# Performance work log

Hardware: AMD Instinct MI355X
Metric: run time of the kernel (lower is better)

The kernel has to match this reference:

```python
import jax, jax.numpy as jnp
import numpy as np

N = 50000      # num_nodes
E = 800000     # num_edges
D = 128        # hidden_dim
POOL_RATIO = 0.5
CROSS_W = 1.0  # cross_weight


def _gcn(x, W, b, src, dst, n):
    """GCNConv: symmetric-normalized aggregation with self-loops. Dropout is identity (eval)."""
    loops = jnp.arange(n)
    s = jnp.concatenate([src, loops])
    d = jnp.concatenate([dst, loops])
    deg = jax.ops.segment_sum(jnp.ones(s.shape, x.dtype), d, num_segments=n)
    inv_sqrt = jax.lax.rsqrt(jnp.maximum(deg, 1.0))  # deg >= 1 due to self-loops
    xw = x @ W                                        # [n, D]
    msg = xw[s] * (inv_sqrt[s] * inv_sqrt[d])[:, None]  # [E+n, D] gather
    return jax.ops.segment_sum(msg, d, num_segments=n) + b


def _prelu(x, a):
    return jnp.where(x >= 0, x, a * x)


def setup_inputs() -> dict:
    key = jax.random.key(0)
    ks = jax.random.split(key, 8)
    glorot = lambda k, sh: jax.random.normal(k, sh, jnp.float32) * np.float32(np.sqrt(2.0 / (sh[0] + sh[1])))
    return {
        "feat": jax.random.normal(ks[0], (N, D), jnp.float32),
        "h_neg": jax.random.normal(ks[1], (N, D), jnp.float32),
        "edge_index": jax.random.randint(ks[2], (2, E), 0, N),
        "Wd": glorot(ks[3], (D, D)),
        "bd": jnp.zeros((D,), jnp.float32),
        "prelu_a": jnp.full((1,), 0.25, jnp.float32),
        "Wbil": glorot(ks[4], (D, D)),
        "bbil": jnp.zeros((1,), jnp.float32),
        "Wg1": glorot(ks[5], (D, D)),
        "bg1": jnp.zeros((D,), jnp.float32),
        "Wg2": glorot(ks[6], (D, D)),
        "bg2": jnp.zeros((D,), jnp.float32),
        "Wg3": glorot(ks[7], (D, D)),
        "bg3": jnp.zeros((D,), jnp.float32),
    }


def reference(feat, h_neg, edge_index, Wd, bd, prelu_a, Wbil, bbil,
              Wg1, bg1, Wg2, bg2, Wg3, bg3):
    src, dst = edge_index[0], edge_index[1]
    # --- IndexSelect: dense layer on pos/neg features ---
    h_pos = _prelu(feat @ Wd + bd, prelu_a)
    h_neg_d = _prelu(h_neg @ Wd + bd, prelu_a)
    embed = _gcn(h_pos, Wg1, bg1, src, dst, N)
    h_center = jax.nn.sigmoid(embed)
    # Discriminator (bilinear) positive scores -> node importance
    score_pos = jnp.einsum('nd,de,ne->n', h_pos, Wbil, h_center) + bbil[0]
    _ = jnp.einsum('nd,de,ne->n', h_neg_d, Wbil, h_center) + bbil[0]  # score_neg (logits branch)
    scores = jax.nn.sigmoid(score_pos)
    order = jnp.argsort(-scores)           # descending
    k = int(POOL_RATIO * N)
    select_idx = order[:k]
    select_scores = scores[order][:k]
    # --- GraphPool (use_gcn=True): down-sample GCN, gather, scale ---
    pooled = _gcn(embed, Wg2, bg2, src, dst, N)[select_idx] * select_scores[:, None]
    # --- GraphUnpool: scatter into zeros, up-sample GCN ---
    fine = jnp.zeros((N, D), feat.dtype).at[select_idx].set(pooled)
    out = _gcn(fine, Wg3, bg3, src, dst, N)
    # --- cross/fuse connection ---
    return out + CROSS_W * embed
```

## Files before the change

### kernel.cpp

```cpp
#include <hip/hip_runtime.h>
#include <hip/hip_bf16.h>

#define NN 50000
#define NE 800000
#define DD 128
#define KSEL 25000
#define NBK 391
#define NBLKA 98

typedef unsigned int uint32;
typedef unsigned short ushort16;

__device__ __forceinline__ float sigmoidf(float x){ return 1.f/(1.f+__expf(-x)); }

__device__ __forceinline__ unsigned short f2b(float f){
  union{float f; unsigned u;} v; v.f=f;
  unsigned r=(v.u + 0x7fffu + ((v.u>>16)&1u))>>16;
  return (unsigned short)r;
}

__device__ __forceinline__ void addbf2(float&lo,float&hi,uint32 u,float w){
  lo+=__uint_as_float(u<<16)*w;
  hi+=__uint_as_float(u&0xffff0000u)*w;
}

__global__ __launch_bounds__(1024) void k_bcount(const int* __restrict__ dst,
    int* __restrict__ btot, int* __restrict__ blkcnt){
  __shared__ int h[NBK];
  int tid=threadIdx.x;
  for(int i=tid;i<NBK;i+=1024) h[i]=0;
  __syncthreads();
  int e0=blockIdx.x*8192;
  #pragma unroll
  for(int t=0;t<8;t++){
    int e=e0+t*1024+tid;
    if(e<NE) atomicAdd(&h[dst[e]>>7],1);
  }
  __syncthreads();
  for(int i=tid;i<NBK;i+=1024){
    int c=h[i];
    blkcnt[blockIdx.x*NBK+i]=c;
    if(c) atomicAdd(&btot[i],c);
  }
}

__global__ __launch_bounds__(512) void k_bscan(const int* __restrict__ btot,
    int* __restrict__ boff, const int* __restrict__ blkcnt, int* __restrict__ blkbase,
    int* __restrict__ row_start){
  __shared__ int sdata[512];
  int tid=threadIdx.x;
  int v=(tid<NBK)?btot[tid]:0;
  sdata[tid]=v; __syncthreads();
  for(int off=1;off<512;off<<=1){
    int y=(tid>=off)?sdata[tid-off]:0;
    __syncthreads();
    sdata[tid]+=y;
    __syncthreads();
  }
  int excl=sdata[tid]-v;
  if(tid<NBK) boff[tid]=excl;
  if(tid==NBK-1){ boff[NBK]=excl+v; row_start[NN]=NE; }
  if(tid<NBK){
    int run=excl;
    for(int b=0;b<NBLKA;b++){
      int c=blkcnt[b*NBK+tid];
      blkbase[b*NBK+tid]=run;
      run+=c;
    }
  }
}

__global__ __launch_bounds__(1024) void k_bscatter(const int* __restrict__ src,
    const int* __restrict__ dst, const int* __restrict__ blkbase, uint2* __restrict__ pairs){
  __shared__ int cur[NBK];
  int tid=threadIdx.x;
  for(int i=tid;i<NBK;i+=1024) cur[i]=blkbase[blockIdx.x*NBK+i];
  __syncthreads();
  int e0=blockIdx.x*8192;
  #pragma unroll
  for(int t=0;t<8;t++){
    int e=e0+t*1024+tid;
    if(e<NE){
      int d=dst[e];
      int p=atomicAdd(&cur[d>>7],1);
      uint2 pr; pr.x=(unsigned)src[e]; pr.y=(unsigned)d;
      pairs[p]=pr;
    }
  }
}

__global__ __launch_bounds__(256) void k_bfinal(const uint2* __restrict__ pairs,
    const int* __restrict__ boff, int* __restrict__ row_start,
    float* __restrict__ inv_sq, int* __restrict__ csr_src){
  __shared__ int degl[128];
  __shared__ int cur[128];
  __shared__ int ssum[2];
  int b=blockIdx.x, tid=threadIdx.x;
  int lo=boff[b], hi=boff[b+1];
  if(tid<128) degl[tid]=0;
  __syncthreads();
  for(int e=lo+tid;e<hi;e+=256) atomicAdd(&degl[pairs[e].y&127],1);
  __syncthreads();
  int v=0,x=0;
  if(tid<128){
    v=degl[tid]; x=v;
    #pragma unroll
    for(int off=1;off<64;off<<=1){
      int y=__shfl_up(x,off,64);
      if((tid&63)>=off) x+=y;
    }
    if((tid&63)==63) ssum[tid>>6]=x;
  }
  __syncthreads();
  if(tid<128){
    int incl=x+((tid>=64)?ssum[0]:0);
    int node=b*128+tid;
    int excl=lo+incl-v;
    if(node<NN){
      row_start[node]=excl;
      cur[tid]=excl;
      inv_sq[node]=1.f/sqrtf((float)(v+1));
    }
  }
  __syncthreads();
  for(int e=lo+tid;e<hi;e+=256){
    uint2 pr=pairs[e];
    int p=atomicAdd(&cur[pr.y&127],1);
    csr_src[p]=(int)pr.x;
  }
}

__global__ void k_transpose(const float* __restrict__ W, float* __restrict__ Wt){
  int idx=blockIdx.x*256+threadIdx.x;
  if(idx<DD*DD){
    int k=idx>>7, c=idx&127;
    Wt[idx]=W[c*DD+k];
  }
}

template<int IN_SIG,int ACT,int OUT_BF16,int FUSE_SCORE>
__global__ __launch_bounds__(256) void k_gemm128(const float* __restrict__ A,
    const float* __restrict__ W, const float* __restrict__ bias,
    float* __restrict__ outf, ushort16* __restrict__ outb,
    const float* __restrict__ aparam, const float* __restrict__ hp,
    const float* __restrict__ bbil, float* __restrict__ score){
  __shared__ float Al[128][132];
  int tid=threadIdx.x;
  int row0=blockIdx.x*128;
  {
    const float4* A4=(const float4*)(A+(size_t)row0*DD);
    #pragma unroll
    for(int i=0;i<16;i++){
      int idx=i*256+tid;
      int r=idx>>5, c=(idx&31)*4;
      float4 v=make_float4(0.f,0.f,0.f,0.f);
      if(row0+r<NN) v=A4[idx];
      if(IN_SIG){ v.x=sigmoidf(v.x); v.y=sigmoidf(v.y); v.z=sigmoidf(v.z); v.w=sigmoidf(v.w); }
      *(float4*)&Al[r][c]=v;
    }
  }
  __syncthreads();
  int tx=tid&15, ty=tid>>4;
  float acc[8][8];
  #pragma unroll
  for(int i=0;i<8;i++)
    #pragma unroll
    for(int c=0;c<8;c++) acc[i][c]=0.f;

  for(int k=0;k<DD;k+=4){
    float wv[4][8];
    #pragma unroll
    for(int r=0;r<4;r++){
      float4 lo=*(const float4*)&W[(size_t)(k+r)*DD+tx*8];
      float4 hi=*(const float4*)&W[(size_t)(k+r)*DD+tx*8+4];
      wv[r][0]=lo.x; wv[r][1]=lo.y; wv[r][2]=lo.z; wv[r][3]=lo.w;
      wv[r][4]=hi.x; wv[r][5]=hi.y; wv[r][6]=hi.z; wv[r][7]=hi.w;
    }
    #pragma unroll
    for(int i=0;i<8;i++){
      float4 a=*(const float4*)&Al[ty+16*i][k];
      #pragma unroll
      for(int c=0;c<8;c++)
        acc[i][c]+=a.x*wv[0][c]+a.y*wv[1][c]+a.z*wv[2][c]+a.w*wv[3][c];
    }
  }

  if(FUSE_SCORE){
    float bb=bbil[0];
    #pragma unroll
    for(int i=0;i<8;i++){
      int r=row0+ty+16*i;
      float p=0.f;
      if(r<NN){
        float4 h0=*(const float4*)&hp[(size_t)r*DD+tx*8];
        float4 h1=*(const float4*)&hp[(size_t)r*DD+tx*8+4];
        p=acc[i][0]*h0.x+acc[i][1]*h0.y+acc[i][2]*h0.z+acc[i][3]*h0.w
         +acc[i][4]*h1.x+acc[i][5]*h1.y+acc[i][6]*h1.z+acc[i][7]*h1.w;
      }
      p+=__shfl_xor(p,1,64); p+=__shfl_xor(p,2,64);
      p+=__shfl_xor(p,4,64); p+=__shfl_xor(p,8,64);
      if(tx==0 && r<NN) score[r]=sigmoidf(p+bb);
    }
    return;
  }
  float bl[8]={0,0,0,0,0,0,0,0};
  if(bias){
    float4 b0=*(const float4*)&bias[tx*8];
    float4 b1=*(const float4*)&bias[tx*8+4];
    bl[0]=b0.x; bl[1]=b0.y; bl[2]=b0.z; bl[3]=b0.w;
    bl[4]=b1.x; bl[5]=b1.y; bl[6]=b1.z; bl[7]=b1.w;
  }
  float ap=ACT?aparam[0]:0.f;
  #pragma unroll
  for(int i=0;i<8;i++){
    int r=row0+ty+16*i;
    if(r<NN){
      float o[8];
      #pragma unroll
      for(int c=0;c<8;c++){
        float t=acc[i][c]+bl[c];
        if(ACT) t=t>=0.f?t:ap*t;
        o[c]=t;
      }
      if(OUT_BF16){
        uint4 pk;
        pk.x=((uint32)f2b(o[1])<<16)|f2b(o[0]);
        pk.y=((uint32)f2b(o[3])<<16)|f2b(o[2]);
        pk.z=((uint32)f2b(o[5])<<16)|f2b(o[4]);
        pk.w=((uint32)f2b(o[7])<<16)|f2b(o[6]);
        *(uint4*)&outb[(size_t)r*DD+tx*8]=pk;
      } else {
        float4 q0; q0.x=o[0]; q0.y=o[1]; q0.z=o[2]; q0.w=o[3];
        float4 q1; q1.x=o[4]; q1.y=o[5]; q1.z=o[6]; q1.w=o[7];
        *(float4*)&outf[(size_t)r*DD+tx*8]=q0;
        *(float4*)&outf[(size_t)r*DD+tx*8+4]=q1;
      }
    }
  }
}

__global__ __launch_bounds__(256) void k_agg_f32(const float* __restrict__ xw,
    const int* __restrict__ row_start, const int* __restrict__ csr,
    const float* __restrict__ inv, const float* __restrict__ bias,
    float* __restrict__ outp){
  int node=blockIdx.x*4+(threadIdx.x>>6);
  if(node>=NN) return;
  int lane=threadIdx.x&63;
  int g=lane>>5, li=lane&31;
  int rs=row_start[node], re=row_start[node+1];
  float a0=0.f,a1=0.f,a2=0.f,a3=0.f;
  int j=rs;
  for(; j+3<re; j+=4){
    int sA=csr[j+g], sB=csr[j+2+g];
    float wA=inv[sA], wB=inv[sB];
    float4 vA=*(const float4*)&xw[(size_t)sA*DD+li*4];
    float4 vB=*(const float4*)&xw[(size_t)sB*DD+li*4];
    a0+=vA.x*wA+vB.x*wB; a1+=vA.y*wA+vB.y*wB;
    a2+=vA.z*wA+vB.z*wB; a3+=vA.w*wA+vB.w*wB;
  }
  for(; j+1<re; j+=2){
    int s=csr[j+g];
    float w=inv[s];
    float4 v=*(const float4*)&xw[(size_t)s*DD+li*4];
    a0+=v.x*w; a1+=v.y*w; a2+=v.z*w; a3+=v.w*w;
  }
  if(j<re && g==0){
    int s=csr[j]; float w=inv[s];
    float4 v=*(const float4*)&xw[(size_t)s*DD+li*4];
    a0+=v.x*w; a1+=v.y*w; a2+=v.z*w; a3+=v.w*w;
  }
  if(g==0){
    float wd=inv[node];
    float4 v=*(const float4*)&xw[(size_t)node*DD+li*4];
    a0+=v.x*wd; a1+=v.y*wd; a2+=v.z*wd; a3+=v.w*wd;
  }
  a0+=__shfl_xor(a0,32,64); a1+=__shfl_xor(a1,32,64);
  a2+=__shfl_xor(a2,32,64); a3+=__shfl_xor(a3,32,64);
  if(g==0){
    float wn=inv[node];
    float4 bv=*(const float4*)&bias[li*4];
    float4 o;
    o.x=a0*wn+bv.x; o.y=a1*wn+bv.y; o.z=a2*wn+bv.z; o.w=a3*wn+bv.w;
    *(float4*)&outp[(size_t)node*DD+li*4]=o;
  }
}

template<int MODE>
__global__ __launch_bounds__(256) void k_agg_b16(const uint32* __restrict__ xwb,
    const int* __restrict__ row_start, const int* __restrict__ csr,
    const float* __restrict__ inv, const float* __restrict__ bias,
    float* __restrict__ outp, const float* __restrict__ score,
    const unsigned char* __restrict__ sel, const float* __restrict__ addbuf){
  int node=blockIdx.x*4+(threadIdx.x>>6);
  if(node>=NN) return;
  int lane=threadIdx.x&63;
  if(MODE==1 && !sel[node]){
    float2 z; z.x=0.f; z.y=0.f;
    *(float2*)&outp[(size_t)node*DD+lane*2]=z;
    return;
  }
  int g=lane>>4, li=lane&15;
  int rs=row_start[node], re=row_start[node+1];
  float a[8];
  #pragma unroll
  for(int c=0;c<8;c++) a[c]=0.f;
  int j=rs;
  for(; j+7<re; j+=8){
    int sA=csr[j+g], sB=csr[j+4+g];
    if(MODE!=2 || sel[sA]){
      float w=inv[sA];
      uint4 u=*(const uint4*)(xwb+(size_t)sA*64+li*4);
      addbf2(a[0],a[1],u.x,w); addbf2(a[2],a[3],u.y,w);
      addbf2(a[4],a[5],u.z,w); addbf2(a[6],a[7],u.w,w);
    }
    if(MODE!=2 || sel[sB]){
      float w=inv[sB];
      uint4 u=*(const uint4*)(xwb+(size_t)sB*64+li*4);
      addbf2(a[0],a[1],u.x,w); addbf2(a[2],a[3],u.y,w);
      addbf2(a[4],a[5],u.z,w); addbf2(a[6],a[7],u.w,w);
    }
  }
  for(; j+3<re; j+=4){
    int s=csr[j+g];
    if(MODE!=2 || sel[s]){
      float w=inv[s];
      uint4 u=*(const uint4*)(xwb+(size_t)s*64+li*4);
      addbf2(a[0],a[1],u.x,w); addbf2(a[2],a[3],u.y,w);
      addbf2(a[4],a[5],u.z,w); addbf2(a[6],a[7],u.w,w);
    }
  }
  int rem=re-j;
  if(g<rem){
    int s=csr[j+g];
    if(MODE!=2 || sel[s]){
      float w=inv[s];
      uint4 u=*(const uint4*)(xwb+(size_t)s*64+li*4);
      addbf2(a[0],a[1],u.x,w); addbf2(a[2],a[3],u.y,w);
      addbf2(a[4],a[5],u.z,w); addbf2(a[6],a[7],u.w,w);
    }
  }
  if(g==0 && (MODE!=2 || sel[node])){
    float wd=inv[node];
    uint4 u=*(const uint4*)(xwb+(size_t)node*64+li*4);
    addbf2(a[0],a[1],u.x,wd); addbf2(a[2],a[3],u.y,wd);
    addbf2(a[4],a[5],u.z,wd); addbf2(a[6],a[7],u.w,wd);
  }
  #pragma unroll
  for(int c=0;c<8;c++){
    a[c]+=__shfl_xor(a[c],16,64);
    a[c]+=__shfl_xor(a[c],32,64);
  }
  if(g<2){
    float wn=inv[node];
    int cb=li*8+g*4;
    float4 bv=*(const float4*)&bias[cb];
    float r0=a[g*4+0]*wn+bv.x, r1=a[g*4+1]*wn+bv.y;
    float r2=a[g*4+2]*wn+bv.z, r3=a[g*4+3]*wn+bv.w;
    if(MODE==1){
      float sc=score[node];
      r0*=sc; r1*=sc; r2*=sc; r3*=sc;
    } else {
      float4 ad=*(const float4*)&addbuf[(size_t)node*DD+cb];
      r0+=ad.x; r1+=ad.y; r2+=ad.z; r3+=ad.w;
    }
    float4 o; o.x=r0; o.y=r1; o.z=r2; o.w=r3;
    *(float4*)&outp[(size_t)node*DD+cb]=o;
  }
}

template<int NB,int PASS>
__global__ __launch_bounds__(256) void k_hist(const float* __restrict__ score,
    int* __restrict__ ghist, const int* __restrict__ ctrl){
  __shared__ int lh[NB];
  int tid=threadIdx.x;
  for(int i=tid;i<NB;i+=256) lh[i]=0;
  __syncthreads();
  int p0=0,p01=0;
  if(PASS==1) p0=ctrl[0];
  if(PASS==2) p01=ctrl[2];
  for(int i=blockIdx.x*256+tid; i<NN; i+=gridDim.x*256){
    unsigned b=__float_as_uint(score[i]);
    if(PASS==0) atomicAdd(&lh[b>>20],1);
    else if(PASS==1){ if((int)(b>>20)==p0) atomicAdd(&lh[(b>>8)&0xFFF],1); }
    else { if((int)(b>>8)==p01) atomicAdd(&lh[b&0xFF],1); }
  }
  __syncthreads();
  for(int i=tid;i<NB;i+=256){ int v=lh[i]; if(v) atomicAdd(&ghist[i],v); }
}

template<int NB,int PASS>
__global__ void k_findb(const int* __restrict__ hist, int* __restrict__ ctrl){
  const int NT=NB/4;
  __shared__ int gsum[NT];
  int t=threadIdx.x;
  int s=hist[t*4]+hist[t*4+1]+hist[t*4+2]+hist[t*4+3];
  int x=s; gsum[t]=x; __syncthreads();
  for(int off=1;off<NT;off<<=1){
    int y=(t+off<NT)?gsum[t+off]:0;
    __syncthreads();
    x+=y; gsum[t]=x; __syncthreads();
  }
  int base;
  if(PASS==0) base=0; else if(PASS==1) base=ctrl[1]; else base=ctrl[3];
  int above=base+((t<NT-1)?gsum[t+1]:0);
  int incl=base+gsum[t];
  if(above<KSEL && incl>=KSEL){
    int c=above, B=0;
    for(int b=3;b>=0;b--){
      int hb=hist[t*4+b];
      if(c+hb>=KSEL){ B=t*4+b; break; }
      c+=hb;
    }
    if(PASS==0){ ctrl[0]=B; ctrl[1]=c; }
    else if(PASS==1){ ctrl[2]=(ctrl[0]<<12)|B; ctrl[3]=c; }
    else { ctrl[4]=(int)((((unsigned)ctrl[2])<<8)|(unsigned)B); ctrl[5]=KSEL-c; }
  }
}

__global__ void k_sel(const float* __restrict__ score, int* __restrict__ ctrl,
                      int* __restrict__ tie_list, unsigned char* __restrict__ sel){
  int i=blockIdx.x*256+threadIdx.x;
  if(i>=NN) return;
  unsigned b=__float_as_uint(score[i]);
  unsigned thr=(unsigned)ctrl[4];
  if(b>thr){ sel[i]=1; }
  else if(b==thr){
    sel[i]=0;
    int p=atomicAdd(&ctrl[6],1);
    if(p<4096) tie_list[p]=i;
  } else sel[i]=0;
}

__global__ __launch_bounds__(256) void k_tie(const int* __restrict__ ctrl,
    const int* __restrict__ tie_list, unsigned char* __restrict__ sel){
  int m=ctrl[6]; if(m>4096) m=4096;
  int needed=ctrl[5];
  for(int t=threadIdx.x; t<m; t+=blockDim.x){
    int idx=tie_list[t];
    int rank=0;
    for(int j=0;j<m;j++) rank+=(tie_list[j]<idx)?1:0;
    if(rank<needed) sel[idx]=1;
  }
}

extern "C" void kernel_launch(void* const* d_in, const int* in_sizes, int n_in,
                              void* d_out, int out_size, void* d_ws, size_t ws_size,
                              hipStream_t stream){
  const float* feat   =(const float*)d_in[0];
  const int*   ei     =(const int*)  d_in[2];
  const int*   src    = ei;
  const int*   dst    = ei + NE;
  const float* Wd     =(const float*)d_in[3];
  const float* bd     =(const float*)d_in[4];
  const float* prelu_a=(const float*)d_in[5];
  const float* Wbil   =(const float*)d_in[6];
  const float* bbil   =(const float*)d_in[7];
  const float* Wg1    =(const float*)d_in[8];
  const float* bg1    =(const float*)d_in[9];
  const float* Wg2    =(const float*)d_in[10];
  const float* bg2    =(const float*)d_in[11];
  const float* Wg3    =(const float*)d_in[12];
  const float* bg3    =(const float*)d_in[13];
  float* out=(float*)d_out;

  char* p=(char*)d_ws;
  auto alloc=[&](size_t bytes)->void*{ void* r=(void*)p; p+=((bytes+255)/256)*256; return r; };
  float* h_pos   =(float*)alloc((size_t)NN*DD*4);
  float* embed   =(float*)alloc((size_t)NN*DD*4);
  float* xw      =(float*)alloc((size_t)NN*DD*4);
  float* score   =(float*)alloc((size_t)NN*4);
  float* inv_sq  =(float*)alloc((size_t)NN*4);
  float* WbT     =(float*)alloc((size_t)DD*DD*4);
  int*   row_st  =(int*)  alloc((size_t)(NN+1)*4);
  int*   csr_src =(int*)  alloc((size_t)NE*4);
  int*   ctrl    =(int*)  alloc(64);
  int*   hist0   =(int*)  alloc(4096*4);
  int*   hist1   =(int*)  alloc(4096*4);
  int*   hist2   =(int*)  alloc(256*4);
  int*   tie_list=(int*)  alloc(4096*4);
  unsigned char* sel=(unsigned char*)alloc(NN);
  int*   btot    =(int*)  alloc((size_t)NBK*4);
  int*   boff    =(int*)  alloc((size_t)(NBK+1)*4);
  int*   blkcnt  =(int*)  alloc((size_t)NBLKA*NBK*4);
  int*   blkbase =(int*)  alloc((size_t)NBLKA*NBK*4);
  uint2* pairs   =(uint2*)xw;
  ushort16* xwb  =(ushort16*)xw;
  float* fine = out;

  const int NB=(NN+255)/256;
  const int GB=(NN+127)/128;
  const int AB=(NN+3)/4;

  hipMemsetAsync(ctrl, 0, (size_t)((char*)tie_list-(char*)ctrl), stream);
  hipMemsetAsync(btot, 0, (size_t)NBK*4, stream);

  k_bcount  <<<NBLKA,1024,0,stream>>>(dst, btot, blkcnt);
  k_bscan   <<<1,512,0,stream>>>(btot, boff, blkcnt, blkbase, row_st);
  k_bscatter<<<NBLKA,1024,0,stream>>>(src, dst, blkbase, pairs);
  k_bfinal  <<<NBK,256,0,stream>>>(pairs, boff, row_st, inv_sq, csr_src);
  k_transpose<<<64,256,0,stream>>>(Wbil, WbT);

  k_gemm128<0,1,0,0><<<GB,256,0,stream>>>(feat, Wd, bd, h_pos, nullptr, prelu_a, nullptr, nullptr, nullptr);
  k_gemm128<0,0,0,0><<<GB,256,0,stream>>>(h_pos, Wg1, nullptr, xw, nullptr, nullptr, nullptr, nullptr, nullptr);
  k_agg_f32<<<AB,256,0,stream>>>(xw, row_st, csr_src, inv_sq, bg1, embed);
  k_gemm128<1,0,0,1><<<GB,256,0,stream>>>(embed, WbT, nullptr, nullptr, nullptr, nullptr, h_pos, bbil, score);
  k_hist<4096,0><<<64,256,0,stream>>>(score, hist0, ctrl);
  k_findb<4096,0><<<1,1024,0,stream>>>(hist0, ctrl);
  k_hist<4096,1><<<64,256,0,stream>>>(score, hist1, ctrl);
  k_findb<4096,1><<<1,1024,0,stream>>>(hist1, ctrl);
  k_hist<256,2><<<64,256,0,stream>>>(score, hist2, ctrl);
  k_findb<256,2><<<1,64,0,stream>>>(hist2, ctrl);
  k_sel<<<NB,256,0,stream>>>(score, ctrl, tie_list, sel);
  k_tie<<<1,256,0,stream>>>(ctrl, tie_list, sel);
  k_gemm128<0,0,1,0><<<GB,256,0,stream>>>(embed, Wg2, nullptr, nullptr, xwb, nullptr, nullptr, nullptr, nullptr);
  k_agg_b16<1><<<AB,256,0,stream>>>((const uint32*)xwb, row_st, csr_src, inv_sq, bg2, fine, score, sel, nullptr);
  k_gemm128<0,0,1,0><<<GB,256,0,stream>>>(fine, Wg3, nullptr, nullptr, xwb, nullptr, nullptr, nullptr, nullptr);
  k_agg_b16<2><<<AB,256,0,stream>>>((const uint32*)xwb, row_st, csr_src, inv_sq, bg3, out, nullptr, sel, embed);
}
```

Baseline: 373.2 us.

## Fuse top-k radix select into one block, pack CSR pairs, unroll f32 aggregation

Replaces the eight-kernel radix-select chain (three histogram passes, three bin finds, select and tie-break) plus a memset with a single 1024-thread block that does all passes in shared memory. This removes launch gaps and global histogram atomics, but it also serialises three scans of 50k scores onto one CU. Edge pairs in the CSR build are packed into 32 bits, src in the low 17 bits and the local dst in the high bits, which halves scatter and read traffic. The f32 aggregation loop is unrolled to eight edges per iteration so more gathers are in flight. The tie buffer shrinks to 2048 entries.

```diff
diff --git a/kernel.cpp b/kernel.cpp
--- a/kernel.cpp
+++ b/kernel.cpp
@@ -71,7 +71,7 @@
 }
 
 __global__ __launch_bounds__(1024) void k_bscatter(const int* __restrict__ src,
-    const int* __restrict__ dst, const int* __restrict__ blkbase, uint2* __restrict__ pairs){
+    const int* __restrict__ dst, const int* __restrict__ blkbase, uint32* __restrict__ pairs){
   __shared__ int cur[NBK];
   int tid=threadIdx.x;
   for(int i=tid;i<NBK;i+=1024) cur[i]=blkbase[blockIdx.x*NBK+i];
@@ -83,13 +83,12 @@
     if(e<NE){
       int d=dst[e];
       int p=atomicAdd(&cur[d>>7],1);
-      uint2 pr; pr.x=(unsigned)src[e]; pr.y=(unsigned)d;
-      pairs[p]=pr;
-    }
-  }
-}
-
-__global__ __launch_bounds__(256) void k_bfinal(const uint2* __restrict__ pairs,
+      pairs[p]=(unsigned)src[e] | ((unsigned)(d&127)<<17);
+    }
+  }
+}
+
+__global__ __launch_bounds__(256) void k_bfinal(const uint32* __restrict__ pairs,
     const int* __restrict__ boff, int* __restrict__ row_start,
     float* __restrict__ inv_sq, int* __restrict__ csr_src){
   __shared__ int degl[128];
@@ -99,7 +98,7 @@
   int lo=boff[b], hi=boff[b+1];
   if(tid<128) degl[tid]=0;
   __syncthreads();
-  for(int e=lo+tid;e<hi;e+=256) atomicAdd(&degl[pairs[e].y&127],1);
+  for(int e=lo+tid;e<hi;e+=256) atomicAdd(&degl[pairs[e]>>17],1);
   __syncthreads();
   int v=0,x=0;
   if(tid<128){
@@ -124,9 +123,9 @@
   }
   __syncthreads();
   for(int e=lo+tid;e<hi;e+=256){
-    uint2 pr=pairs[e];
-    int p=atomicAdd(&cur[pr.y&127],1);
-    csr_src[p]=(int)pr.x;
+    uint32 u=pairs[e];
+    int p=atomicAdd(&cur[u>>17],1);
+    csr_src[p]=(int)(u&0x1FFFFu);
   }
 }
 
@@ -250,13 +249,17 @@
   int rs=row_start[node], re=row_start[node+1];
   float a0=0.f,a1=0.f,a2=0.f,a3=0.f;
   int j=rs;
-  for(; j+3<re; j+=4){
-    int sA=csr[j+g], sB=csr[j+2+g];
-    float wA=inv[sA], wB=inv[sB];
-    float4 vA=*(const float4*)&xw[(size_t)sA*DD+li*4];
-    float4 vB=*(const float4*)&xw[(size_t)sB*DD+li*4];
-    a0+=vA.x*wA+vB.x*wB; a1+=vA.y*wA+vB.y*wB;
-    a2+=vA.z*wA+vB.z*wB; a3+=vA.w*wA+vB.w*wB;
+  for(; j+7<re; j+=8){
+    int s0=csr[j+g], s1=csr[j+2+g], s2=csr[j+4+g], s3=csr[j+6+g];
+    float w0=inv[s0], w1=inv[s1], w2=inv[s2], w3=inv[s3];
+    float4 v0=*(const float4*)&xw[(size_t)s0*DD+li*4];
+    float4 v1=*(const float4*)&xw[(size_t)s1*DD+li*4];
+    float4 v2=*(const float4*)&xw[(size_t)s2*DD+li*4];
+    float4 v3=*(const float4*)&xw[(size_t)s3*DD+li*4];
+    a0+=v0.x*w0+v1.x*w1+v2.x*w2+v3.x*w3;
+    a1+=v0.y*w0+v1.y*w1+v2.y*w2+v3.y*w3;
+    a2+=v0.z*w0+v1.z*w1+v2.z*w2+v3.z*w3;
+    a3+=v0.w*w0+v1.w*w1+v2.w*w2+v3.w*w3;
   }
   for(; j+1<re; j+=2){
     int s=csr[j+g];
@@ -368,77 +371,107 @@
   }
 }
 
-template<int NB,int PASS>
-__global__ __launch_bounds__(256) void k_hist(const float* __restrict__ score,
-    int* __restrict__ ghist, const int* __restrict__ ctrl){
-  __shared__ int lh[NB];
+__global__ __launch_bounds__(1024) void k_select(const float* __restrict__ score,
+    unsigned char* __restrict__ sel){
+  __shared__ int h[4096];
+  __shared__ int gs[1024];
+  __shared__ int tie[2048];
+  __shared__ int st[8];
   int tid=threadIdx.x;
-  for(int i=tid;i<NB;i+=256) lh[i]=0;
-  __syncthreads();
-  int p0=0,p01=0;
-  if(PASS==1) p0=ctrl[0];
-  if(PASS==2) p01=ctrl[2];
-  for(int i=blockIdx.x*256+tid; i<NN; i+=gridDim.x*256){
+  if(tid==0) st[6]=0;
+  for(int i=tid;i<4096;i+=1024) h[i]=0;
+  __syncthreads();
+  for(int i=tid;i<NN;i+=1024){
     unsigned b=__float_as_uint(score[i]);
-    if(PASS==0) atomicAdd(&lh[b>>20],1);
-    else if(PASS==1){ if((int)(b>>20)==p0) atomicAdd(&lh[(b>>8)&0xFFF],1); }
-    else { if((int)(b>>8)==p01) atomicAdd(&lh[b&0xFF],1); }
-  }
-  __syncthreads();
-  for(int i=tid;i<NB;i+=256){ int v=lh[i]; if(v) atomicAdd(&ghist[i],v); }
-}
-
-template<int NB,int PASS>
-__global__ void k_findb(const int* __restrict__ hist, int* __restrict__ ctrl){
-  const int NT=NB/4;
-  __shared__ int gsum[NT];
-  int t=threadIdx.x;
-  int s=hist[t*4]+hist[t*4+1]+hist[t*4+2]+hist[t*4+3];
-  int x=s; gsum[t]=x; __syncthreads();
-  for(int off=1;off<NT;off<<=1){
-    int y=(t+off<NT)?gsum[t+off]:0;
-    __syncthreads();
-    x+=y; gsum[t]=x; __syncthreads();
-  }
-  int base;
-  if(PASS==0) base=0; else if(PASS==1) base=ctrl[1]; else base=ctrl[3];
-  int above=base+((t<NT-1)?gsum[t+1]:0);
-  int incl=base+gsum[t];
-  if(above<KSEL && incl>=KSEL){
-    int c=above, B=0;
-    for(int b=3;b>=0;b--){
-      int hb=hist[t*4+b];
-      if(c+hb>=KSEL){ B=t*4+b; break; }
-      c+=hb;
-    }
-    if(PASS==0){ ctrl[0]=B; ctrl[1]=c; }
-    else if(PASS==1){ ctrl[2]=(ctrl[0]<<12)|B; ctrl[3]=c; }
-    else { ctrl[4]=(int)((((unsigned)ctrl[2])<<8)|(unsigned)B); ctrl[5]=KSEL-c; }
-  }
-}
-
-__global__ void k_sel(const float* __restrict__ score, int* __restrict__ ctrl,
-                      int* __restrict__ tie_list, unsigned char* __restrict__ sel){
-  int i=blockIdx.x*256+threadIdx.x;
-  if(i>=NN) return;
-  unsigned b=__float_as_uint(score[i]);
-  unsigned thr=(unsigned)ctrl[4];
-  if(b>thr){ sel[i]=1; }
-  else if(b==thr){
-    sel[i]=0;
-    int p=atomicAdd(&ctrl[6],1);
-    if(p<4096) tie_list[p]=i;
-  } else sel[i]=0;
-}
-
-__global__ __launch_bounds__(256) void k_tie(const int* __restrict__ ctrl,
-    const int* __restrict__ tie_list, unsigned char* __restrict__ sel){
-  int m=ctrl[6]; if(m>4096) m=4096;
-  int needed=ctrl[5];
-  for(int t=threadIdx.x; t<m; t+=blockDim.x){
-    int idx=tie_list[t];
+    atomicAdd(&h[b>>20],1);
+  }
+  __syncthreads();
+  {
+    int s=h[tid*4]+h[tid*4+1]+h[tid*4+2]+h[tid*4+3];
+    int x=s; gs[tid]=x; __syncthreads();
+    for(int off=1;off<1024;off<<=1){
+      int y=(tid+off<1024)?gs[tid+off]:0;
+      __syncthreads(); x+=y; gs[tid]=x; __syncthreads();
+    }
+    int incl=x, above=x-s;
+    if(above<KSEL && incl>=KSEL){
+      int c=above, B=0;
+      for(int b=3;b>=0;b--){ int hb=h[tid*4+b]; if(c+hb>=KSEL){B=tid*4+b;break;} c+=hb; }
+      st[0]=B; st[1]=c;
+    }
+  }
+  __syncthreads();
+  int B0=st[0];
+  for(int i=tid;i<4096;i+=1024) h[i]=0;
+  __syncthreads();
+  for(int i=tid;i<NN;i+=1024){
+    unsigned b=__float_as_uint(score[i]);
+    if((int)(b>>20)==B0) atomicAdd(&h[(b>>8)&0xFFF],1);
+  }
+  __syncthreads();
+  {
+    int base=st[1];
+    int s=h[tid*4]+h[tid*4+1]+h[tid*4+2]+h[tid*4+3];
+    int x=s; gs[tid]=x; __syncthreads();
+    for(int off=1;off<1024;off<<=1){
+      int y=(tid+off<1024)?gs[tid+off]:0;
+      __syncthreads(); x+=y; gs[tid]=x; __syncthreads();
+    }
+    int incl=base+x, above=base+x-s;
+    if(above<KSEL && incl>=KSEL){
+      int c=above, B=0;
+      for(int b=3;b>=0;b--){ int hb=h[tid*4+b]; if(c+hb>=KSEL){B=tid*4+b;break;} c+=hb; }
+      st[2]=(B0<<12)|B; st[3]=c;
+    }
+  }
+  __syncthreads();
+  int P01=st[2];
+  for(int i=tid;i<256;i+=1024) h[i]=0;
+  __syncthreads();
+  for(int i=tid;i<NN;i+=1024){
+    unsigned b=__float_as_uint(score[i]);
+    if((int)(b>>8)==P01) atomicAdd(&h[b&0xFF],1);
+  }
+  __syncthreads();
+  {
+    int base=st[3];
+    int s=0,x=0;
+    if(tid<64){ s=h[tid*4]+h[tid*4+1]+h[tid*4+2]+h[tid*4+3]; x=s; }
+    gs[tid]=x; __syncthreads();
+    for(int off=1;off<64;off<<=1){
+      int y=(tid+off<64)?gs[tid+off]:0;
+      __syncthreads();
+      if(tid<64){ x+=y; gs[tid]=x; }
+      __syncthreads();
+    }
+    if(tid<64){
+      int incl=base+x, above=base+x-s;
+      if(above<KSEL && incl>=KSEL){
+        int c=above, B=0;
+        for(int b=3;b>=0;b--){ int hb=h[tid*4+b]; if(c+hb>=KSEL){B=tid*4+b;break;} c+=hb; }
+        st[4]=(int)((((unsigned)P01)<<8)|(unsigned)B); st[5]=KSEL-c;
+      }
+    }
+  }
+  __syncthreads();
+  unsigned thr=(unsigned)st[4];
+  for(int i=tid;i<NN;i+=1024){
+    unsigned b=__float_as_uint(score[i]);
+    unsigned char sv=0;
+    if(b>thr) sv=1;
+    else if(b==thr){
+      int p=atomicAdd(&st[6],1);
+      if(p<2048) tie[p]=i;
+    }
+    sel[i]=sv;
+  }
+  __syncthreads();
+  int m=st[6]; if(m>2048) m=2048;
+  int needed=st[5];
+  for(int t=tid;t<m;t+=1024){
+    int idx=tie[t];
     int rank=0;
-    for(int j=0;j<m;j++) rank+=(tie_list[j]<idx)?1:0;
+    for(int j2=0;j2<m;j2++) rank+=(tie[j2]<idx)?1:0;
     if(rank<needed) sel[idx]=1;
   }
 }
@@ -473,25 +506,18 @@
   float* WbT     =(float*)alloc((size_t)DD*DD*4);
   int*   row_st  =(int*)  alloc((size_t)(NN+1)*4);
   int*   csr_src =(int*)  alloc((size_t)NE*4);
-  int*   ctrl    =(int*)  alloc(64);
-  int*   hist0   =(int*)  alloc(4096*4);
-  int*   hist1   =(int*)  alloc(4096*4);
-  int*   hist2   =(int*)  alloc(256*4);
-  int*   tie_list=(int*)  alloc(4096*4);
   unsigned char* sel=(unsigned char*)alloc(NN);
   int*   btot    =(int*)  alloc((size_t)NBK*4);
   int*   boff    =(int*)  alloc((size_t)(NBK+1)*4);
   int*   blkcnt  =(int*)  alloc((size_t)NBLKA*NBK*4);
   int*   blkbase =(int*)  alloc((size_t)NBLKA*NBK*4);
-  uint2* pairs   =(uint2*)xw;
+  uint32* pairs  =(uint32*)xw;
   ushort16* xwb  =(ushort16*)xw;
   float* fine = out;
 
-  const int NB=(NN+255)/256;
   const int GB=(NN+127)/128;
   const int AB=(NN+3)/4;
 
-  hipMemsetAsync(ctrl, 0, (size_t)((char*)tie_list-(char*)ctrl), stream);
   hipMemsetAsync(btot, 0, (size_t)NBK*4, stream);
 
   k_bcount  <<<NBLKA,1024,0,stream>>>(dst, btot, blkcnt);
@@ -504,14 +530,7 @@
   k_gemm128<0,0,0,0><<<GB,256,0,stream>>>(h_pos, Wg1, nullptr, xw, nullptr, nullptr, nullptr, nullptr, nullptr);
   k_agg_f32<<<AB,256,0,stream>>>(xw, row_st, csr_src, inv_sq, bg1, embed);
   k_gemm128<1,0,0,1><<<GB,256,0,stream>>>(embed, WbT, nullptr, nullptr, nullptr, nullptr, h_pos, bbil, score);
-  k_hist<4096,0><<<64,256,0,stream>>>(score, hist0, ctrl);
-  k_findb<4096,0><<<1,1024,0,stream>>>(hist0, ctrl);
-  k_hist<4096,1><<<64,256,0,stream>>>(score, hist1, ctrl);
-  k_findb<4096,1><<<1,1024,0,stream>>>(hist1, ctrl);
-  k_hist<256,2><<<64,256,0,stream>>>(score, hist2, ctrl);
-  k_findb<256,2><<<1,64,0,stream>>>(hist2, ctrl);
-  k_sel<<<NB,256,0,stream>>>(score, ctrl, tie_list, sel);
-  k_tie<<<1,256,0,stream>>>(ctrl, tie_list, sel);
+  k_select<<<1,1024,0,stream>>>(score, sel);
   k_gemm128<0,0,1,0><<<GB,256,0,stream>>>(embed, Wg2, nullptr, nullptr, xwb, nullptr, nullptr, nullptr, nullptr);
   k_agg_b16<1><<<AB,256,0,stream>>>((const uint32*)xwb, row_st, csr_src, inv_sq, bg2, fine, score, sel, nullptr);
   k_gemm128<0,0,1,0><<<GB,256,0,stream>>>(fine, Wg3, nullptr, nullptr, xwb, nullptr, nullptr, nullptr, nullptr);
```

Result: slower. 394.5 us (+5.7%).

## Pack CSR build pairs, shrink GEMM row tile to 96, unroll f32 aggregation

Applied to the files above, without the earlier changes.

Three separate changes. The bucket-scatter pairs shrink from two 32-bit words to one, packing the source index in the low 17 bits and the low 7 bits of the destination above them, which halves the scratch traffic during the CSR build. The 128-dim GEMM now takes 96 rows per block instead of 128 (6 accumulator rows per thread), giving more blocks and less shared memory and register use per block for better occupancy, at the cost of more redundant W reads. The f32 aggregation loop issues 8 edges per iteration instead of 4 for more memory-level parallelism.

```diff
diff --git a/kernel.cpp b/kernel.cpp
--- a/kernel.cpp
+++ b/kernel.cpp
@@ -71,7 +71,7 @@
 }
 
 __global__ __launch_bounds__(1024) void k_bscatter(const int* __restrict__ src,
-    const int* __restrict__ dst, const int* __restrict__ blkbase, uint2* __restrict__ pairs){
+    const int* __restrict__ dst, const int* __restrict__ blkbase, uint32* __restrict__ pairs){
   __shared__ int cur[NBK];
   int tid=threadIdx.x;
   for(int i=tid;i<NBK;i+=1024) cur[i]=blkbase[blockIdx.x*NBK+i];
@@ -83,13 +83,12 @@
     if(e<NE){
       int d=dst[e];
       int p=atomicAdd(&cur[d>>7],1);
-      uint2 pr; pr.x=(unsigned)src[e]; pr.y=(unsigned)d;
-      pairs[p]=pr;
-    }
-  }
-}
-
-__global__ __launch_bounds__(256) void k_bfinal(const uint2* __restrict__ pairs,
+      pairs[p]=(unsigned)src[e] | ((unsigned)(d&127)<<17);
+    }
+  }
+}
+
+__global__ __launch_bounds__(256) void k_bfinal(const uint32* __restrict__ pairs,
     const int* __restrict__ boff, int* __restrict__ row_start,
     float* __restrict__ inv_sq, int* __restrict__ csr_src){
   __shared__ int degl[128];
@@ -99,7 +98,7 @@
   int lo=boff[b], hi=boff[b+1];
   if(tid<128) degl[tid]=0;
   __syncthreads();
-  for(int e=lo+tid;e<hi;e+=256) atomicAdd(&degl[pairs[e].y&127],1);
+  for(int e=lo+tid;e<hi;e+=256) atomicAdd(&degl[pairs[e]>>17],1);
   __syncthreads();
   int v=0,x=0;
   if(tid<128){
@@ -124,9 +123,9 @@
   }
   __syncthreads();
   for(int e=lo+tid;e<hi;e+=256){
-    uint2 pr=pairs[e];
-    int p=atomicAdd(&cur[pr.y&127],1);
-    csr_src[p]=(int)pr.x;
+    uint32 u=pairs[e];
+    int p=atomicAdd(&cur[u>>17],1);
+    csr_src[p]=(int)(u&0x1FFFFu);
   }
 }
 
@@ -139,18 +138,18 @@
 }
 
 template<int IN_SIG,int ACT,int OUT_BF16,int FUSE_SCORE>
-__global__ __launch_bounds__(256) void k_gemm128(const float* __restrict__ A,
+__global__ __launch_bounds__(256) void k_gemm96(const float* __restrict__ A,
     const float* __restrict__ W, const float* __restrict__ bias,
     float* __restrict__ outf, ushort16* __restrict__ outb,
     const float* __restrict__ aparam, const float* __restrict__ hp,
     const float* __restrict__ bbil, float* __restrict__ score){
-  __shared__ float Al[128][132];
+  __shared__ float Al[96][132];
   int tid=threadIdx.x;
-  int row0=blockIdx.x*128;
+  int row0=blockIdx.x*96;
   {
     const float4* A4=(const float4*)(A+(size_t)row0*DD);
     #pragma unroll
-    for(int i=0;i<16;i++){
+    for(int i=0;i<12;i++){
       int idx=i*256+tid;
       int r=idx>>5, c=(idx&31)*4;
       float4 v=make_float4(0.f,0.f,0.f,0.f);
@@ -161,9 +160,9 @@
   }
   __syncthreads();
   int tx=tid&15, ty=tid>>4;
-  float acc[8][8];
+  float acc[6][8];
   #pragma unroll
-  for(int i=0;i<8;i++)
+  for(int i=0;i<6;i++)
     #pragma unroll
     for(int c=0;c<8;c++) acc[i][c]=0.f;
 
@@ -177,7 +176,7 @@
       wv[r][4]=hi.x; wv[r][5]=hi.y; wv[r][6]=hi.z; wv[r][7]=hi.w;
     }
     #pragma unroll
-    for(int i=0;i<8;i++){
+    for(int i=0;i<6;i++){
       float4 a=*(const float4*)&Al[ty+16*i][k];
       #pragma unroll
       for(int c=0;c<8;c++)
@@ -188,7 +187,7 @@
   if(FUSE_SCORE){
     float bb=bbil[0];
     #pragma unroll
-    for(int i=0;i<8;i++){
+    for(int i=0;i<6;i++){
       int r=row0+ty+16*i;
       float p=0.f;
       if(r<NN){
@@ -212,7 +211,7 @@
   }
   float ap=ACT?aparam[0]:0.f;
   #pragma unroll
-  for(int i=0;i<8;i++){
+  for(int i=0;i<6;i++){
     int r=row0+ty+16*i;
     if(r<NN){
       float o[8];
@@ -250,13 +249,17 @@
   int rs=row_start[node], re=row_start[node+1];
   float a0=0.f,a1=0.f,a2=0.f,a3=0.f;
   int j=rs;
-  for(; j+3<re; j+=4){
-    int sA=csr[j+g], sB=csr[j+2+g];
-    float wA=inv[sA], wB=inv[sB];
-    float4 vA=*(const float4*)&xw[(size_t)sA*DD+li*4];
-    float4 vB=*(const float4*)&xw[(size_t)sB*DD+li*4];
-    a0+=vA.x*wA+vB.x*wB; a1+=vA.y*wA+vB.y*wB;
-    a2+=vA.z*wA+vB.z*wB; a3+=vA.w*wA+vB.w*wB;
+  for(; j+7<re; j+=8){
+    int s0=csr[j+g], s1=csr[j+2+g], s2=csr[j+4+g], s3=csr[j+6+g];
+    float w0=inv[s0], w1=inv[s1], w2=inv[s2], w3=inv[s3];
+    float4 v0=*(const float4*)&xw[(size_t)s0*DD+li*4];
+    float4 v1=*(const float4*)&xw[(size_t)s1*DD+li*4];
+    float4 v2=*(const float4*)&xw[(size_t)s2*DD+li*4];
+    float4 v3=*(const float4*)&xw[(size_t)s3*DD+li*4];
+    a0+=v0.x*w0+v1.x*w1+v2.x*w2+v3.x*w3;
+    a1+=v0.y*w0+v1.y*w1+v2.y*w2+v3.y*w3;
+    a2+=v0.z*w0+v1.z*w1+v2.z*w2+v3.z*w3;
+    a3+=v0.w*w0+v1.w*w1+v2.w*w2+v3.w*w3;
   }
   for(; j+1<re; j+=2){
     int s=csr[j+g];
@@ -483,12 +486,12 @@
   int*   boff    =(int*)  alloc((size_t)(NBK+1)*4);
   int*   blkcnt  =(int*)  alloc((size_t)NBLKA*NBK*4);
   int*   blkbase =(int*)  alloc((size_t)NBLKA*NBK*4);
-  uint2* pairs   =(uint2*)xw;
+  uint32* pairs  =(uint32*)xw;
   ushort16* xwb  =(ushort16*)xw;
   float* fine = out;
 
   const int NB=(NN+255)/256;
-  const int GB=(NN+127)/128;
+  const int GB=(NN+95)/96;
   const int AB=(NN+3)/4;
 
   hipMemsetAsync(ctrl, 0, (size_t)((char*)tie_list-(char*)ctrl), stream);
@@ -500,10 +503,10 @@
   k_bfinal  <<<NBK,256,0,stream>>>(pairs, boff, row_st, inv_sq, csr_src);
   k_transpose<<<64,256,0,stream>>>(Wbil, WbT);
 
-  k_gemm128<0,1,0,0><<<GB,256,0,stream>>>(feat, Wd, bd, h_pos, nullptr, prelu_a, nullptr, nullptr, nullptr);
-  k_gemm128<0,0,0,0><<<GB,256,0,stream>>>(h_pos, Wg1, nullptr, xw, nullptr, nullptr, nullptr, nullptr, nullptr);
+  k_gemm96<0,1,0,0><<<GB,256,0,stream>>>(feat, Wd, bd, h_pos, nullptr, prelu_a, nullptr, nullptr, nullptr);
+  k_gemm96<0,0,0,0><<<GB,256,0,stream>>>(h_pos, Wg1, nullptr, xw, nullptr, nullptr, nullptr, nullptr, nullptr);
   k_agg_f32<<<AB,256,0,stream>>>(xw, row_st, csr_src, inv_sq, bg1, embed);
-  k_gemm128<1,0,0,1><<<GB,256,0,stream>>>(embed, WbT, nullptr, nullptr, nullptr, nullptr, h_pos, bbil, score);
+  k_gemm96<1,0,0,1><<<GB,256,0,stream>>>(embed, WbT, nullptr, nullptr, nullptr, nullptr, h_pos, bbil, score);
   k_hist<4096,0><<<64,256,0,stream>>>(score, hist0, ctrl);
   k_findb<4096,0><<<1,1024,0,stream>>>(hist0, ctrl);
   k_hist<4096,1><<<64,256,0,stream>>>(score, hist1, ctrl);
@@ -512,8 +515,8 @@
   k_findb<256,2><<<1,64,0,stream>>>(hist2, ctrl);
   k_sel<<<NB,256,0,stream>>>(score, ctrl, tie_list, sel);
   k_tie<<<1,256,0,stream>>>(ctrl, tie_list, sel);
-  k_gemm128<0,0,1,0><<<GB,256,0,stream>>>(embed, Wg2, nullptr, nullptr, xwb, nullptr, nullptr, nullptr, nullptr);
+  k_gemm96<0,0,1,0><<<GB,256,0,stream>>>(embed, Wg2, nullptr, nullptr, xwb, nullptr, nullptr, nullptr, nullptr);
   k_agg_b16<1><<<AB,256,0,stream>>>((const uint32*)xwb, row_st, csr_src, inv_sq, bg2, fine, score, sel, nullptr);
-  k_gemm128<0,0,1,0><<<GB,256,0,stream>>>(fine, Wg3, nullptr, nullptr, xwb, nullptr, nullptr, nullptr, nullptr);
+  k_gemm96<0,0,1,0><<<GB,256,0,stream>>>(fine, Wg3, nullptr, nullptr, xwb, nullptr, nullptr, nullptr, nullptr);
   k_agg_b16<2><<<AB,256,0,stream>>>((const uint32*)xwb, row_st, csr_src, inv_sq, bg3, out, nullptr, sel, embed);
 }
```

After: 371.7 us. Within noise of the previous version (-0.4%).
